# Performance work log

Measured on AMD Instinct MI355X. Metric: run time of the kernel, lower is better.

The kernel has to match this reference:

```python
import jax, jax.numpy as jnp
import numpy as np

N, F, D, R, E = 1024, 256, 64, 11, 2048
ALPHA = 0.2  # LeakyReLU negative slope


def setup_inputs() -> dict:
    key = jax.random.key(0)
    k1, k2, k3, k4, k5, k6 = jax.random.split(key, 6)
    x = jax.random.normal(k1, (N, F), dtype=jnp.float32)
    # Relation-specific weights (ParameterList of [F, D]) stacked: [R, F, D]
    W = jax.random.normal(k2, (R, F, D), dtype=jnp.float32) * (1.414 * (6.0 / (F + D)) ** 0.5)
    # nn.Linear(2*D, 1, bias=False) weight as a vector [2*D]
    a = jax.random.normal(k3, (2 * D,), dtype=jnp.float32) * (1.0 / (2 * D) ** 0.5)
    src_idx = jax.random.randint(k4, (E,), 0, N, dtype=jnp.int32)
    dst_idx = jax.random.randint(k5, (E,), 0, N, dtype=jnp.int32)
    rel_idx = jax.random.randint(k6, (E,), 0, R, dtype=jnp.int32)
    return {"x": x, "W": W, "a": a, "src_idx": src_idx, "dst_idx": dst_idx, "rel_idx": rel_idx}


def reference(x, W, a, src_idx, dst_idx, rel_idx):
    # Per-edge relation weight gather: [E, F, D]
    We = W[rel_idx]
    # einsum('i,ij->ij', emb, W) == row-wise scaling of W by the embedding
    nt = x[dst_idx][:, :, None] * We          # neighbour_temp: [E, F, D]
    ft = x[src_idx][:, :, None] * We          # feature_temp:   [E, F, D]
    hh = jnp.concatenate([ft, nt], axis=-1)   # [E, F, 2D]
    # linear(2D -> 1, no bias) then LeakyReLU: [E, F]
    e = jax.nn.leaky_relu(jnp.einsum('efd,d->ef', hh, a), ALPHA)
    # original: attn = softmax over edge dim (dim=1 of [F, E]); here edges are axis 0
    attn = jax.nn.softmax(e, axis=0)          # [E, F]
    # h[e] = attn[:, e, None] * nt[e]; cat over edges along dim=1 then sum over F
    # => per edge: sum_F attn[e, f] * nt[e, f, :] -> [E, D], flattened to [E*D]
    out = jnp.einsum('ef,efd->ed', attn, nt).reshape(-1)
    return out
```

## Files before the change

kernel.cpp:

```cpp
#include <hip/hip_runtime.h>
#include <hip/hip_bf16.h>

#define NN 1024
#define FF 256
#define DD 64
#define RR 11
#define EE 2048
#define ALPHA 0.2f
#define TPB 512
#define EPT (EE / TPB)
#define PERM_CAP 2176
#define K2_GRID (PERM_CAP / 8)


__global__ __launch_bounds__(TPB) void k1_coef(
    const float* __restrict__ x, const float* __restrict__ W,
    const float* __restrict__ a, const int* __restrict__ src,
    const int* __restrict__ dst, const int* __restrict__ rel,
    float* __restrict__ cbuf, int* __restrict__ perm,
    int* __restrict__ ntiles_p) {

    const int b    = blockIdx.x;
    const int f    = ((b & 7) << 5) | (b >> 3);
    const int tid  = threadIdx.x;
    const int wid  = tid >> 6;
    const int lane = tid & 63;

    __shared__ float xcol[NN];
    __shared__ float p_sh[RR], q_sh[RR];
    __shared__ float red_s[8];
    __shared__ int   hist[16], off_sh[16];

    for (int i = tid; i < NN; i += TPB) xcol[i] = x[(size_t)i * FF + f];

    for (int r = wid; r < RR; r += 8) {
        float w  = W[((size_t)r * FF + f) * DD + lane];
        float pa = w * a[lane];
        float qa = w * a[DD + lane];
        #pragma unroll
        for (int o = 32; o > 0; o >>= 1) {
            pa += __shfl_down(pa, o);
            qa += __shfl_down(qa, o);
        }
        if (lane == 0) { p_sh[r] = pa; q_sh[r] = qa; }
    }
    __syncthreads();

    float uvals[EPT];
    float s = 0.0f;
    #pragma unroll
    for (int k = 0; k < EPT; ++k) {
        int e = tid + k * TPB;
        float xs = xcol[src[e]];
        float xd = xcol[dst[e]];
        int r = rel[e];
        float v = xs * p_sh[r] + xd * q_sh[r];
        v = v > 0.0f ? v : ALPHA * v;
        float ev = expf(v);
        uvals[k] = ev * xd;
        s += ev;
    }
    #pragma unroll
    for (int o = 32; o > 0; o >>= 1) s += __shfl_down(s, o);
    if (lane == 0) red_s[wid] = s;
    __syncthreads();
    float st = red_s[0];
    #pragma unroll
    for (int i = 1; i < 8; ++i) st += red_s[i];
    float inv = 1.0f / st;

    #pragma unroll
    for (int k = 0; k < EPT; ++k) {
        int e = tid + k * TPB;
        cbuf[(size_t)e * FF + f] = uvals[k] * inv;
    }

    if (b == 0) {
        if (tid < 16) hist[tid] = 0;
        __syncthreads();
        for (int e = tid; e < EE; e += TPB) atomicAdd(&hist[rel[e]], 1);
        __syncthreads();
        if (tid == 0) {
            int acc = 0;
            for (int r = 0; r < RR; ++r) {
                off_sh[r] = acc;
                acc += (hist[r] + 7) & ~7;
            }
            *ntiles_p = acc >> 3;
        }
        __syncthreads();
        for (int i = tid; i < PERM_CAP; i += TPB) perm[i] = -1;
        __syncthreads();
        for (int e = tid; e < EE; e += TPB) {
            int pos = atomicAdd(&off_sh[rel[e]], 1);
            perm[pos] = e;
        }
    }
}

__global__ __launch_bounds__(TPB) void k2_out(
    const float* __restrict__ W, const int* __restrict__ rel,
    const float* __restrict__ cbuf, const int* __restrict__ perm,
    const int* __restrict__ ntiles_p, float* __restrict__ out) {

    const int b = blockIdx.x;
    const int t = (b & 7) * 34 + (b >> 3);
    if (t >= *ntiles_p) return;

    const int tid  = threadIdx.x;
    const int wid  = tid >> 6;
    const int lane = tid & 63;

    __shared__ float Wl[32 * DD];
    __shared__ int   e_sh[8], r_sh;

    if (tid < 8) e_sh[tid] = perm[t * 8 + tid];
    __syncthreads();
    if (tid == 0) {
        int rr = 0;
        #pragma unroll
        for (int i = 7; i >= 0; --i) if (e_sh[i] >= 0) rr = rel[e_sh[i]];
        r_sh = rr;
    }
    __syncthreads();

    const int e = e_sh[wid];
    const float* __restrict__ Wr = W + (size_t)r_sh * FF * DD;
    const float* __restrict__ ce = (e >= 0) ? (cbuf + (size_t)e * FF) : cbuf;

    const int fg = lane >> 4;
    const int dq = lane & 15;
    const int srow = tid >> 4;
    const int scol = tid & 15;

    float4 nxt = *(const float4*)&Wr[(size_t)srow * DD + scol * 4];

    float4 acc = make_float4(0.f, 0.f, 0.f, 0.f);
    #pragma unroll
    for (int fc = 0; fc < FF / 32; ++fc) {
        __syncthreads();
        *(float4*)&Wl[srow * DD + scol * 4] = nxt;
        __syncthreads();
        if (fc < FF / 32 - 1)
            nxt = *(const float4*)
                &Wr[(size_t)((fc + 1) * 32 + srow) * DD + scol * 4];
        if (e >= 0) {
            #pragma unroll
            for (int j = 0; j < 8; ++j) {
                int lf = j * 4 + fg;
                float c = ce[fc * 32 + lf];
                float4 w4 = *(const float4*)&Wl[lf * DD + dq * 4];
                acc.x = fmaf(c, w4.x, acc.x);
                acc.y = fmaf(c, w4.y, acc.y);
                acc.z = fmaf(c, w4.z, acc.z);
                acc.w = fmaf(c, w4.w, acc.w);
            }
        }
    }

    #pragma unroll
    for (int o = 16; o <= 32; o <<= 1) {
        acc.x += __shfl_xor(acc.x, o);
        acc.y += __shfl_xor(acc.y, o);
        acc.z += __shfl_xor(acc.z, o);
        acc.w += __shfl_xor(acc.w, o);
    }
    if (e >= 0 && fg == 0)
        *(float4*)&out[(size_t)e * DD + dq * 4] = acc;
}

extern "C" void kernel_launch(void* const* d_in, const int* in_sizes, int n_in,
                              void* d_out, int out_size, void* d_ws, size_t ws_size,
                              hipStream_t stream) {
    const float* x  = (const float*)d_in[0];
    const float* W  = (const float*)d_in[1];
    const float* a  = (const float*)d_in[2];
    const int* src  = (const int*)d_in[3];
    const int* dst  = (const int*)d_in[4];
    const int* rel  = (const int*)d_in[5];
    float* out      = (float*)d_out;

    char* wsb = (char*)d_ws;
    int*   ntiles_p = (int*)wsb;
    int*   perm     = (int*)(wsb + 256);
    float* cbuf     = (float*)(wsb + 16384);

    k1_coef<<<FF, TPB, 0, stream>>>(x, W, a, src, dst, rel,
                                    cbuf, perm, ntiles_p);
    k2_out<<<K2_GRID, TPB, 0, stream>>>(W, rel, cbuf, perm, ntiles_p, out);
}
```

Measured before the change: 21.52 us.

## Recompute edge coefficients in output kernel instead of materializing cbuf

The first kernel now stores only per-feature softmax inverse denominators and the per-relation p/q projections. It no longer writes the full E×F coefficient buffer. The second kernel recomputes each coefficient on the fly from the x rows of src and dst, which removes a 2 MB write and read round trip. The permutation build moves to a dedicated extra block so it no longer serializes inside block 0, and the first kernel gathers x directly instead of staging a column in shared memory. The cost is redundant expf work and uncoalesced x gathers in the output kernel.

```diff
diff --git a/kernel.cpp b/kernel.cpp
--- a/kernel.cpp
+++ b/kernel.cpp
@@ -13,25 +13,47 @@
 #define K2_GRID (PERM_CAP / 8)
 
 
-__global__ __launch_bounds__(TPB) void k1_coef(
+__global__ __launch_bounds__(TPB) void k1_stats(
     const float* __restrict__ x, const float* __restrict__ W,
     const float* __restrict__ a, const int* __restrict__ src,
     const int* __restrict__ dst, const int* __restrict__ rel,
-    float* __restrict__ cbuf, int* __restrict__ perm,
+    float* __restrict__ pT, float* __restrict__ qT,
+    float* __restrict__ inv, int* __restrict__ perm,
     int* __restrict__ ntiles_p) {
 
     const int b    = blockIdx.x;
-    const int f    = ((b & 7) << 5) | (b >> 3);
     const int tid  = threadIdx.x;
     const int wid  = tid >> 6;
     const int lane = tid & 63;
 
-    __shared__ float xcol[NN];
     __shared__ float p_sh[RR], q_sh[RR];
     __shared__ float red_s[8];
     __shared__ int   hist[16], off_sh[16];
 
-    for (int i = tid; i < NN; i += TPB) xcol[i] = x[(size_t)i * FF + f];
+    if (b == FF) {
+        if (tid < 16) hist[tid] = 0;
+        __syncthreads();
+        for (int e = tid; e < EE; e += TPB) atomicAdd(&hist[rel[e]], 1);
+        __syncthreads();
+        if (tid == 0) {
+            int acc = 0;
+            for (int r = 0; r < RR; ++r) {
+                off_sh[r] = acc;
+                acc += (hist[r] + 7) & ~7;
+            }
+            *ntiles_p = acc >> 3;
+        }
+        __syncthreads();
+        for (int i = tid; i < PERM_CAP; i += TPB) perm[i] = -1;
+        __syncthreads();
+        for (int e = tid; e < EE; e += TPB) {
+            int pos = atomicAdd(&off_sh[rel[e]], 1);
+            perm[pos] = e;
+        }
+        return;
+    }
+
+    const int f = ((b & 7) << 5) | (b >> 3);
 
     for (int r = wid; r < RR; r += 8) {
         float w  = W[((size_t)r * FF + f) * DD + lane];
@@ -42,23 +64,32 @@
             pa += __shfl_down(pa, o);
             qa += __shfl_down(qa, o);
         }
-        if (lane == 0) { p_sh[r] = pa; q_sh[r] = qa; }
+        if (lane == 0) {
+            p_sh[r] = pa; q_sh[r] = qa;
+            pT[r * FF + f] = pa;
+            qT[r * FF + f] = qa;
+        }
     }
     __syncthreads();
 
-    float uvals[EPT];
-    float s = 0.0f;
+    int siA[EPT], diA[EPT], rA[EPT];
     #pragma unroll
     for (int k = 0; k < EPT; ++k) {
         int e = tid + k * TPB;
-        float xs = xcol[src[e]];
-        float xd = xcol[dst[e]];
-        int r = rel[e];
-        float v = xs * p_sh[r] + xd * q_sh[r];
+        siA[k] = src[e]; diA[k] = dst[e]; rA[k] = rel[e];
+    }
+    float xsA[EPT], xdA[EPT];
+    #pragma unroll
+    for (int k = 0; k < EPT; ++k) {
+        xsA[k] = x[(size_t)siA[k] * FF + f];
+        xdA[k] = x[(size_t)diA[k] * FF + f];
+    }
+    float s = 0.0f;
+    #pragma unroll
+    for (int k = 0; k < EPT; ++k) {
+        float v = xsA[k] * p_sh[rA[k]] + xdA[k] * q_sh[rA[k]];
         v = v > 0.0f ? v : ALPHA * v;
-        float ev = expf(v);
-        uvals[k] = ev * xd;
-        s += ev;
+        s += expf(v);
     }
     #pragma unroll
     for (int o = 32; o > 0; o >>= 1) s += __shfl_down(s, o);
@@ -67,40 +98,15 @@
     float st = red_s[0];
     #pragma unroll
     for (int i = 1; i < 8; ++i) st += red_s[i];
-    float inv = 1.0f / st;
-
-    #pragma unroll
-    for (int k = 0; k < EPT; ++k) {
-        int e = tid + k * TPB;
-        cbuf[(size_t)e * FF + f] = uvals[k] * inv;
-    }
-
-    if (b == 0) {
-        if (tid < 16) hist[tid] = 0;
-        __syncthreads();
-        for (int e = tid; e < EE; e += TPB) atomicAdd(&hist[rel[e]], 1);
-        __syncthreads();
-        if (tid == 0) {
-            int acc = 0;
-            for (int r = 0; r < RR; ++r) {
-                off_sh[r] = acc;
-                acc += (hist[r] + 7) & ~7;
-            }
-            *ntiles_p = acc >> 3;
-        }
-        __syncthreads();
-        for (int i = tid; i < PERM_CAP; i += TPB) perm[i] = -1;
-        __syncthreads();
-        for (int e = tid; e < EE; e += TPB) {
-            int pos = atomicAdd(&off_sh[rel[e]], 1);
-            perm[pos] = e;
-        }
-    }
+    if (tid == 0) inv[f] = 1.0f / st;
 }
 
 __global__ __launch_bounds__(TPB) void k2_out(
-    const float* __restrict__ W, const int* __restrict__ rel,
-    const float* __restrict__ cbuf, const int* __restrict__ perm,
+    const float* __restrict__ x, const float* __restrict__ W,
+    const int* __restrict__ src, const int* __restrict__ dst,
+    const int* __restrict__ rel,
+    const float* __restrict__ pT, const float* __restrict__ qT,
+    const float* __restrict__ inv, const int* __restrict__ perm,
     const int* __restrict__ ntiles_p, float* __restrict__ out) {
 
     const int b = blockIdx.x;
@@ -112,21 +118,22 @@
     const int lane = tid & 63;
 
     __shared__ float Wl[32 * DD];
-    __shared__ int   e_sh[8], r_sh;
+    __shared__ float p_l[FF], q_l[FF], iv_l[FF];
+    __shared__ int   e_sh[8];
 
     if (tid < 8) e_sh[tid] = perm[t * 8 + tid];
     __syncthreads();
-    if (tid == 0) {
-        int rr = 0;
-        #pragma unroll
-        for (int i = 7; i >= 0; --i) if (e_sh[i] >= 0) rr = rel[e_sh[i]];
-        r_sh = rr;
-    }
-    __syncthreads();
+
+    const int r = rel[e_sh[0]];
+    const size_t rb = (size_t)r * FF;
+    if (tid < FF) { p_l[tid] = pT[rb + tid]; iv_l[tid] = inv[tid]; }
+    else          { q_l[tid - FF] = qT[rb + tid - FF]; }
 
     const int e = e_sh[wid];
-    const float* __restrict__ Wr = W + (size_t)r_sh * FF * DD;
-    const float* __restrict__ ce = (e >= 0) ? (cbuf + (size_t)e * FF) : cbuf;
+    const int es = (e >= 0) ? e : 0;
+    const float* __restrict__ xrs = x + (size_t)src[es] * FF;
+    const float* __restrict__ xrd = x + (size_t)dst[es] * FF;
+    const float* __restrict__ Wr  = W + rb * DD;
 
     const int fg = lane >> 4;
     const int dq = lane & 15;
@@ -148,7 +155,12 @@
             #pragma unroll
             for (int j = 0; j < 8; ++j) {
                 int lf = j * 4 + fg;
-                float c = ce[fc * 32 + lf];
+                int gf = fc * 32 + lf;
+                float xs = xrs[gf];
+                float xd = xrd[gf];
+                float v = xs * p_l[gf] + xd * q_l[gf];
+                v = v > 0.0f ? v : ALPHA * v;
+                float c = expf(v) * iv_l[gf] * xd;
                 float4 w4 = *(const float4*)&Wl[lf * DD + dq * 4];
                 acc.x = fmaf(c, w4.x, acc.x);
                 acc.y = fmaf(c, w4.y, acc.y);
@@ -183,9 +195,12 @@
     char* wsb = (char*)d_ws;
     int*   ntiles_p = (int*)wsb;
     int*   perm     = (int*)(wsb + 256);
-    float* cbuf     = (float*)(wsb + 16384);
-
-    k1_coef<<<FF, TPB, 0, stream>>>(x, W, a, src, dst, rel,
-                                    cbuf, perm, ntiles_p);
-    k2_out<<<K2_GRID, TPB, 0, stream>>>(W, rel, cbuf, perm, ntiles_p, out);
+    float* inv      = (float*)(wsb + 12288);
+    float* pT       = (float*)(wsb + 16384);
+    float* qT       = (float*)(wsb + 32768);
+
+    k1_stats<<<FF + 1, TPB, 0, stream>>>(x, W, a, src, dst, rel,
+                                         pT, qT, inv, perm, ntiles_p);
+    k2_out<<<K2_GRID, TPB, 0, stream>>>(x, W, src, dst, rel, pT, qT, inv,
+                                        perm, ntiles_p, out);
 }
```

New measurement: 27.09 us. 25.9% more time.

## Process 32 edges per block in output kernel to reuse staged W tile

Applied to the files above, without the earlier changes.

Raises the per-block edge tile in the second kernel from 8 to 32 edges of the same relation, with each wave handling 4 edges. Every W row staged in LDS is now used by four edges per wave, so LDS and global W traffic per edge goes down. The costs are more padding per relation (PERM_CAP grows), fewer blocks (76 instead of 272), and fewer waves in flight to hide latency on a GPU with many CUs. The relation is now read directly from the first edge of each tile.

```diff
diff --git a/kernel.cpp b/kernel.cpp
--- a/kernel.cpp
+++ b/kernel.cpp
@@ -9,8 +9,9 @@
 #define ALPHA 0.2f
 #define TPB 512
 #define EPT (EE / TPB)
-#define PERM_CAP 2176
-#define K2_GRID (PERM_CAP / 8)
+#define TILE_E 32
+#define PERM_CAP 2432
+#define K2_GRID (PERM_CAP / TILE_E)
 
 
 __global__ __launch_bounds__(TPB) void k1_coef(
@@ -84,9 +85,9 @@
             int acc = 0;
             for (int r = 0; r < RR; ++r) {
                 off_sh[r] = acc;
-                acc += (hist[r] + 7) & ~7;
+                acc += (hist[r] + TILE_E - 1) & ~(TILE_E - 1);
             }
-            *ntiles_p = acc >> 3;
+            *ntiles_p = acc / TILE_E;
         }
         __syncthreads();
         for (int i = tid; i < PERM_CAP; i += TPB) perm[i] = -1;
@@ -103,8 +104,7 @@
     const float* __restrict__ cbuf, const int* __restrict__ perm,
     const int* __restrict__ ntiles_p, float* __restrict__ out) {
 
-    const int b = blockIdx.x;
-    const int t = (b & 7) * 34 + (b >> 3);
+    const int t = blockIdx.x;
     if (t >= *ntiles_p) return;
 
     const int tid  = threadIdx.x;
@@ -112,21 +112,23 @@
     const int lane = tid & 63;
 
     __shared__ float Wl[32 * DD];
-    __shared__ int   e_sh[8], r_sh;
+    __shared__ int   e_sh[TILE_E];
 
-    if (tid < 8) e_sh[tid] = perm[t * 8 + tid];
-    __syncthreads();
-    if (tid == 0) {
-        int rr = 0;
-        #pragma unroll
-        for (int i = 7; i >= 0; --i) if (e_sh[i] >= 0) rr = rel[e_sh[i]];
-        r_sh = rr;
-    }
+    if (tid < TILE_E) e_sh[tid] = perm[t * TILE_E + tid];
     __syncthreads();
 
-    const int e = e_sh[wid];
-    const float* __restrict__ Wr = W + (size_t)r_sh * FF * DD;
-    const float* __restrict__ ce = (e >= 0) ? (cbuf + (size_t)e * FF) : cbuf;
+    const int r = rel[e_sh[0]];
+    const float* __restrict__ Wr = W + (size_t)r * FF * DD;
+
+    int eb[4];
+    const float* ce[4];
+    float4 acc[4];
+    #pragma unroll
+    for (int j = 0; j < 4; ++j) {
+        eb[j]  = e_sh[wid * 4 + j];
+        ce[j]  = cbuf + (size_t)(eb[j] >= 0 ? eb[j] : 0) * FF;
+        acc[j] = make_float4(0.f, 0.f, 0.f, 0.f);
+    }
 
     const int fg = lane >> 4;
     const int dq = lane & 15;
@@ -135,7 +137,6 @@
 
     float4 nxt = *(const float4*)&Wr[(size_t)srow * DD + scol * 4];
 
-    float4 acc = make_float4(0.f, 0.f, 0.f, 0.f);
     #pragma unroll
     for (int fc = 0; fc < FF / 32; ++fc) {
         __syncthreads();
@@ -144,29 +145,34 @@
         if (fc < FF / 32 - 1)
             nxt = *(const float4*)
                 &Wr[(size_t)((fc + 1) * 32 + srow) * DD + scol * 4];
-        if (e >= 0) {
+        #pragma unroll
+        for (int i = 0; i < 8; ++i) {
+            int lf = i * 4 + fg;
+            float4 w4 = *(const float4*)&Wl[lf * DD + dq * 4];
+            int gf = fc * 32 + lf;
             #pragma unroll
-            for (int j = 0; j < 8; ++j) {
-                int lf = j * 4 + fg;
-                float c = ce[fc * 32 + lf];
-                float4 w4 = *(const float4*)&Wl[lf * DD + dq * 4];
-                acc.x = fmaf(c, w4.x, acc.x);
-                acc.y = fmaf(c, w4.y, acc.y);
-                acc.z = fmaf(c, w4.z, acc.z);
-                acc.w = fmaf(c, w4.w, acc.w);
+            for (int j = 0; j < 4; ++j) {
+                float c = ce[j][gf];
+                acc[j].x = fmaf(c, w4.x, acc[j].x);
+                acc[j].y = fmaf(c, w4.y, acc[j].y);
+                acc[j].z = fmaf(c, w4.z, acc[j].z);
+                acc[j].w = fmaf(c, w4.w, acc[j].w);
             }
         }
     }
 
     #pragma unroll
-    for (int o = 16; o <= 32; o <<= 1) {
-        acc.x += __shfl_xor(acc.x, o);
-        acc.y += __shfl_xor(acc.y, o);
-        acc.z += __shfl_xor(acc.z, o);
-        acc.w += __shfl_xor(acc.w, o);
+    for (int j = 0; j < 4; ++j) {
+        #pragma unroll
+        for (int o = 16; o <= 32; o <<= 1) {
+            acc[j].x += __shfl_xor(acc[j].x, o);
+            acc[j].y += __shfl_xor(acc[j].y, o);
+            acc[j].z += __shfl_xor(acc[j].z, o);
+            acc[j].w += __shfl_xor(acc[j].w, o);
+        }
+        if (eb[j] >= 0 && fg == 0)
+            *(float4*)&out[(size_t)eb[j] * DD + dq * 4] = acc[j];
     }
-    if (e >= 0 && fg == 0)
-        *(float4*)&out[(size_t)e * DD + dq * 4] = acc;
 }
 
 extern "C" void kernel_launch(void* const* d_in, const int* in_sizes, int n_in,
```

New measurement: 21.68 us. No clear change (+0.8%).
